# Kernel optimization log

Measured on AMD Instinct MI355X. Metric: run time of the kernel, lower is better.

## Reference

```python
import jax, jax.numpy as jnp
import numpy as np

NINP = 512
NHEAD = 8


def setup_inputs() -> dict:
    key = jax.random.key(0)
    ks = jax.random.split(key, 7)
    B, M, L, C = 2, 32, 512, NINP
    s = 1.0 / np.sqrt(C)
    return {
        "x": jax.random.normal(ks[0], (B, M, L, C), dtype=jnp.float32),
        "Wq": jax.random.normal(ks[1], (C, C), dtype=jnp.float32) * s,
        "bq": jax.random.normal(ks[2], (C,), dtype=jnp.float32) * s,
        "Wk": jax.random.normal(ks[3], (C, C), dtype=jnp.float32) * s,
        "bk": jax.random.normal(ks[4], (C,), dtype=jnp.float32) * s,
        "Wv": jax.random.normal(ks[5], (C, C), dtype=jnp.float32) * s,
        "bv": jax.random.normal(ks[6], (C,), dtype=jnp.float32) * s,
    }


def reference(x, Wq, bq, Wk, bk, Wv, bv) -> jnp.ndarray:
    # x: (B, M, L, C). Attention over L within each (B, M) block.
    B, M, L, C = x.shape
    H = NHEAD
    D = C // H
    scale = 1.0 / jnp.sqrt(jnp.asarray(D, dtype=x.dtype))

    def split_heads(t):  # (B,M,L,C) -> (B,M,H,L,D)
        return t.reshape(B, M, L, H, D).transpose(0, 1, 3, 2, 4)

    q = split_heads(x @ Wq + bq)
    k = split_heads(x @ Wk + bk)
    v = split_heads(x @ Wv + bv)

    scores = jnp.einsum("bmhid,bmhjd->bmhij", q, k) * scale
    w = jax.nn.softmax(scores, axis=-1)  # dropout p=0 -> identity
    out = jnp.einsum("bmhij,bmhjd->bmhid", w, v)  # (B,M,H,L,D)
    return out.transpose(0, 1, 3, 2, 4).reshape(B, M, L, C)
```

## Files before the change

### kernel.cpp

```cpp
#include <hip/hip_runtime.h>


typedef unsigned short u16;
typedef unsigned int u32;
typedef unsigned long long u64;
typedef __bf16 bf16x8 __attribute__((ext_vector_type(8)));
typedef float f32x4 __attribute__((ext_vector_type(4)));

#define SCQ 0.18033688011112042f

static __device__ __forceinline__ u16 f2bf(float f) {
  u32 x = __float_as_uint(f);
  x += 0x7fffu + ((x >> 16) & 1u);
  return (u16)(x >> 16);
}

static __device__ __forceinline__ u32 pkbf(float f0, float f1) {
  return __builtin_amdgcn_perm(__float_as_uint(f1) + 0x8000u,
                               __float_as_uint(f0) + 0x8000u, 0x07060302u);
}

typedef __attribute__((address_space(1))) const void* gvp;
typedef __attribute__((address_space(3))) void* lvp;
static __device__ __forceinline__ void glds16(const void* g, void* l) {
  __builtin_amdgcn_global_load_lds((gvp)g, (lvp)l, 16, 0, 0);
}

__global__ __launch_bounds__(256) void prep(const float* __restrict__ x,
                                            u16* __restrict__ xb,
                                            const float* __restrict__ Wq,
                                            const float* __restrict__ Wk,
                                            const float* __restrict__ Wv,
                                            u16* __restrict__ WT) {
  __shared__ float t[32][33];
  const int bx = blockIdx.x;
  if (bx < 8192) {
    const u32 i = (bx * 256u + threadIdx.x) * 8u;
    const float4 a = *(const float4*)(x + i);
    const float4 b = *(const float4*)(x + i + 4);
    union { u16 r[8]; uint4 v; } u;
    u.r[0] = f2bf(a.x); u.r[1] = f2bf(a.y); u.r[2] = f2bf(a.z); u.r[3] = f2bf(a.w);
    u.r[4] = f2bf(b.x); u.r[5] = f2bf(b.y); u.r[6] = f2bf(b.z); u.r[7] = f2bf(b.w);
    *(uint4*)(xb + i) = u.v;
    return;
  }
  const int b = bx - 8192;
  const int z = b >> 8;
  const int rem = b & 255;
  const float* W = (z == 0) ? Wq : ((z == 1) ? Wk : Wv);
  u16* dst = WT + z * 262144;
  const int k0 = (rem >> 4) * 32, n0 = (rem & 15) * 32;
  const int tx = threadIdx.x & 31, ty = threadIdx.x >> 5;
#pragma unroll
  for (int i = 0; i < 32; i += 8)
    t[ty + i][tx] = W[(size_t)(k0 + ty + i) * 512 + n0 + tx];
  __syncthreads();
#pragma unroll
  for (int i = 0; i < 32; i += 8)
    dst[(size_t)(n0 + ty + i) * 512 + k0 + tx] = f2bf(t[tx][ty + i]);
}

__global__ __launch_bounds__(256) void gemm_qkv(const u16* __restrict__ xb,
                                                const u16* __restrict__ WT,
                                                const float* __restrict__ bq,
                                                const float* __restrict__ bk,
                                                const float* __restrict__ bv,
                                                u16* __restrict__ qkv) {
  __shared__ __align__(16) u16 smem[24576];
  const int id = blockIdx.x;
  const int xcd = id & 7;
  const int slot = id >> 3;
  const int r12 = slot % 12;
  const int z = r12 >> 2;
  const int m = (slot / 12) * 8 + xcd;
  const int mbase = m * 128;
  const int nbase = (r12 & 3) * 128;
  const u16* Bg = WT + z * 262144;
  const float* bias = (z == 0) ? bq : ((z == 1) ? bk : bv);
  u16* out = qkv + (size_t)z * 16777216u;
  const int tid = threadIdx.x;
  const int lane = tid & 63;
  const int w = tid >> 6;
  const int wy = w >> 1, wx = w & 1;
  const int m15 = lane & 15, g = lane >> 4;

  const int srow = w * 32 + (lane >> 2);
  const int scol = (lane & 3) * 8;
  const u16* Ap = xb + (size_t)(mbase + srow) * 512 + scol;
  const u16* Bp = Bg + (size_t)(nbase + srow) * 512 + scol;

  f32x4 acc[4][4] = {};

#define STAGE(KT, B)                                  \
  do {                                                \
    const int k0_ = (KT) * 32;                        \
    u16* d_ = (B) + w * 1024;                         \
    glds16(Ap + k0_, d_);                             \
    glds16(Ap + k0_ + 16 * 512, d_ + 512);            \
    glds16(Bp + k0_, d_ + 4096);                      \
    glds16(Bp + k0_ + 16 * 512, d_ + 4096 + 512);     \
  } while (0)

#define COMPUTE(B)                                                          \
  do {                                                                      \
    bf16x8 af[4], bfr[4];                                                   \
    _Pragma("unroll") for (int t = 0; t < 4; ++t)                           \
        af[t] = *(const bf16x8*)&(B)[(wy * 64 + t * 16 + m15) * 32 + g * 8];\
    _Pragma("unroll") for (int t = 0; t < 4; ++t)                           \
        bfr[t] = *(const bf16x8*)&(B)[4096 + (wx * 64 + t * 16 + m15) * 32 + g * 8]; \
    _Pragma("unroll") for (int rt = 0; rt < 4; ++rt)                        \
        _Pragma("unroll") for (int ct = 0; ct < 4; ++ct)                    \
            acc[rt][ct] = __builtin_amdgcn_mfma_f32_16x16x32_bf16(          \
                af[rt], bfr[ct], acc[rt][ct], 0, 0, 0);                     \
  } while (0)

  STAGE(0, smem);
  STAGE(1, smem + 8192);
  STAGE(2, smem + 16384);

#pragma unroll
  for (int kt = 0; kt < 16; ++kt) {
    u16* cb = smem + (kt % 3) * 8192;
    if (kt < 14)
      asm volatile("s_waitcnt vmcnt(8)" ::: "memory");
    else if (kt == 14)
      asm volatile("s_waitcnt vmcnt(4)" ::: "memory");
    else
      asm volatile("s_waitcnt vmcnt(0)" ::: "memory");
    __builtin_amdgcn_s_barrier();
    COMPUTE(cb);
    asm volatile("s_waitcnt lgkmcnt(0)" ::: "memory");
    __builtin_amdgcn_s_barrier();
    if (kt + 3 < 16) STAGE(kt + 3, cb);
  }
#undef STAGE
#undef COMPUTE

  if (z < 2) {
    const float sc = (z == 0) ? SCQ : 1.0f;
#pragma unroll
    for (int ct = 0; ct < 4; ++ct) {
      const int col = nbase + wx * 64 + ct * 16 + m15;
      const float bb = bias[col];
#pragma unroll
      for (int rt = 0; rt < 4; ++rt) {
        const int row0 = mbase + wy * 64 + rt * 16 + g * 4;
#pragma unroll
        for (int r = 0; r < 4; ++r)
          out[(size_t)(row0 + r) * 512 + col] = f2bf((acc[rt][ct][r] + bb) * sc);
      }
    }
  } else {
    const int bm = mbase >> 9, jb = mbase & 511;
    u16* sT = smem;
#pragma unroll
    for (int cn = 0; cn < 4; ++cn) {
      __syncthreads();
      if (wx == (cn >> 1)) {
#pragma unroll
        for (int cte = 0; cte < 2; ++cte) {
          const int ct = (cn & 1) * 2 + cte;
          const int ncol = nbase + wx * 64 + ct * 16 + m15;
          const float bb = bias[ncol];
          const int nl = cte * 16 + m15;
#pragma unroll
          for (int rt = 0; rt < 4; ++rt) {
            u64 pk = 0;
#pragma unroll
            for (int r = 0; r < 4; ++r)
              pk |= (u64)f2bf(acc[rt][ct][r] + bb) << (16 * r);
            *(u64*)&sT[nl * 136 + wy * 64 + rt * 16 + g * 4] = pk;
          }
        }
      }
      __syncthreads();
#pragma unroll
      for (int it = 0; it < 2; ++it) {
        const int nl = it * 16 + (tid >> 4);
        const int ml = (tid & 15) * 8;
        const int ng = nbase + cn * 32 + nl;
        const int h = ng >> 6, d = ng & 63;
        *(uint4*)(out + ((size_t)((bm * 8 + h) * 64 + d)) * 512 + jb + ml) =
            *(const uint4*)&sT[nl * 136 + ml];
      }
    }
  }
}

__global__ __launch_bounds__(256) void attn(const u16* __restrict__ Q,
                                            const u16* __restrict__ K,
                                            const u16* __restrict__ Vt,
                                            float* __restrict__ out) {
  __shared__ __align__(16) char smem[36864];
  u16* sK = (u16*)smem;
  u16* sVT = (u16*)(smem + 9216);
  const int tid = threadIdx.x;
  const int lane = tid & 63;
  const int w = tid >> 6;
  const int m15 = lane & 15, g = lane >> 4;
  const int qt = blockIdx.x, h = blockIdx.y, bm = blockIdx.z;
  const size_t rb = (size_t)bm * 512;
  const int q0 = qt * 128 + w * 32;
  u16* sPT = (u16*)(smem + 18432) + w * 2304;

  bf16x8 qf[2][2];
#pragma unroll
  for (int ct = 0; ct < 2; ++ct)
#pragma unroll
    for (int kc = 0; kc < 2; ++kc)
      qf[ct][kc] =
          *(const bf16x8*)(Q + (rb + q0 + ct * 16 + m15) * 512 + h * 64 + kc * 32 + g * 8);

  f32x4 acc[4][2] = {};
  f32x4 lv[2] = {};

  const int srow = tid >> 3, sc8 = (tid & 7) * 8;
  const u16* Kb = K + rb * 512 + h * 64;
  const u16* Vtb = Vt + (size_t)(bm * 8 + h) * 64 * 512;

  uint4 k0v = *(const uint4*)(Kb + (size_t)srow * 512 + sc8);
  uint4 k1v = *(const uint4*)(Kb + (size_t)(srow + 32) * 512 + sc8);
  uint4 v0v = *(const uint4*)(Vtb + (size_t)srow * 512 + sc8);
  uint4 v1v = *(const uint4*)(Vtb + (size_t)(srow + 32) * 512 + sc8);

  for (int jt = 0; jt < 8; ++jt) {
    asm volatile("s_waitcnt lgkmcnt(0)" ::: "memory");
    __builtin_amdgcn_s_barrier();
    asm volatile("s_waitcnt vmcnt(0)" ::: "memory");
    *(uint4*)&sK[srow * 72 + sc8] = k0v;
    *(uint4*)&sK[(srow + 32) * 72 + sc8] = k1v;
    *(uint4*)&sVT[srow * 72 + sc8] = v0v;
    *(uint4*)&sVT[(srow + 32) * 72 + sc8] = v1v;
    if (jt < 7) {
      const int j1 = (jt + 1) * 64;
      k0v = *(const uint4*)(Kb + (size_t)(j1 + srow) * 512 + sc8);
      k1v = *(const uint4*)(Kb + (size_t)(j1 + srow + 32) * 512 + sc8);
      v0v = *(const uint4*)(Vtb + (size_t)srow * 512 + j1 + sc8);
      v1v = *(const uint4*)(Vtb + (size_t)(srow + 32) * 512 + j1 + sc8);
    }
    asm volatile("s_waitcnt lgkmcnt(0)" ::: "memory");
    __builtin_amdgcn_s_barrier();

    f32x4 s[4][2];
#pragma unroll
    for (int rt = 0; rt < 4; ++rt) {
      const bf16x8 k0 = *(const bf16x8*)&sK[(rt * 16 + m15) * 72 + g * 8];
      const bf16x8 k1 = *(const bf16x8*)&sK[(rt * 16 + m15) * 72 + 32 + g * 8];
#pragma unroll
      for (int ct = 0; ct < 2; ++ct) {
        f32x4 z = {};
        z = __builtin_amdgcn_mfma_f32_16x16x32_bf16(k0, qf[ct][0], z, 0, 0, 0);
        s[rt][ct] = __builtin_amdgcn_mfma_f32_16x16x32_bf16(k1, qf[ct][1], z, 0, 0, 0);
      }
    }

#pragma unroll
    for (int ct = 0; ct < 2; ++ct)
#pragma unroll
      for (int rt = 0; rt < 4; ++rt) {
        f32x4 p;
#pragma unroll
        for (int r = 0; r < 4; ++r) p[r] = exp2f(s[rt][ct][r]);
        lv[ct] += p;
        uint2 pk = {pkbf(p[0], p[1]), pkbf(p[2], p[3])};
        *(uint2*)&sPT[(ct * 16 + m15) * 72 + rt * 16 + g * 4] = pk;
      }

    bf16x8 pb[2][2];
#pragma unroll
    for (int ct = 0; ct < 2; ++ct)
#pragma unroll
      for (int kc = 0; kc < 2; ++kc)
        pb[ct][kc] = *(const bf16x8*)&sPT[(ct * 16 + m15) * 72 + kc * 32 + g * 8];
#pragma unroll
    for (int dt = 0; dt < 4; ++dt) {
      const bf16x8 v0 = *(const bf16x8*)&sVT[(dt * 16 + m15) * 72 + g * 8];
      const bf16x8 v1 = *(const bf16x8*)&sVT[(dt * 16 + m15) * 72 + 32 + g * 8];
#pragma unroll
      for (int ct = 0; ct < 2; ++ct) {
        acc[dt][ct] = __builtin_amdgcn_mfma_f32_16x16x32_bf16(v0, pb[ct][0], acc[dt][ct], 0, 0, 0);
        acc[dt][ct] = __builtin_amdgcn_mfma_f32_16x16x32_bf16(v1, pb[ct][1], acc[dt][ct], 0, 0, 0);
      }
    }
  }

  float inv[2];
#pragma unroll
  for (int ct = 0; ct < 2; ++ct) {
    float l = lv[ct][0] + lv[ct][1] + lv[ct][2] + lv[ct][3];
    l += __shfl_xor(l, 16);
    l += __shfl_xor(l, 32);
    inv[ct] = 1.0f / l;
  }
  __syncthreads();
  float* sO = (float*)(smem + w * 4608);
#pragma unroll
  for (int c = 0; c < 2; ++c) {
#pragma unroll
    for (int dt2 = 0; dt2 < 2; ++dt2)
#pragma unroll
      for (int ct = 0; ct < 2; ++ct) {
        f32x4 v = acc[c * 2 + dt2][ct] * inv[ct];
        *(f32x4*)&sO[(ct * 16 + m15) * 36 + dt2 * 16 + g * 4] = v;
      }
#pragma unroll
    for (int it = 0; it < 4; ++it) {
      const int q = it * 8 + (lane >> 3);
      f32x4 v = *(const f32x4*)&sO[q * 36 + (lane & 7) * 4];
      *(f32x4*)&out[(rb + q0 + q) * 512 + h * 64 + c * 32 + (lane & 7) * 4] = v;
    }
  }
}

extern "C" void kernel_launch(void* const* d_in, const int* in_sizes, int n_in,
                              void* d_out, int out_size, void* d_ws, size_t ws_size,
                              hipStream_t stream) {
  const float* x = (const float*)d_in[0];
  const float* Wq = (const float*)d_in[1];
  const float* bq = (const float*)d_in[2];
  const float* Wk = (const float*)d_in[3];
  const float* bk = (const float*)d_in[4];
  const float* Wv = (const float*)d_in[5];
  const float* bv = (const float*)d_in[6];
  float* out = (float*)d_out;

  u16* ws = (u16*)d_ws;
  u16* xb = ws;
  u16* WT = ws + 16777216;
  u16* qkv = ws + 17563648;

  prep<<<8960, 256, 0, stream>>>(x, xb, Wq, Wk, Wv, WT);
  gemm_qkv<<<3072, 256, 0, stream>>>(xb, WT, bq, bk, bv, qkv);
  attn<<<dim3(4, 8, 64), 256, 0, stream>>>(qkv, qkv + 16777216, qkv + 2 * 16777216, out);
}
```

Before: 256.0 us.

## Quad-buffer QKV GEMM, compute softmax sums via MFMA, remap attention grid

The QKV GEMM moves from three to four LDS stages, so the next tile's prefetch can be issued before compute and one barrier per k-step is dropped. In attention, the softmax row sums come from an MFMA against a ones vector on the bf16 probabilities instead of per-lane vector adds and cross-lane shuffles. The bf16 packing now uses the hardware v_cvt_pk_bf16_f32 instruction, and a 1D grid maps heads to adjacent block ids for better L2 locality on K and V. The costs are more LDS per GEMM block, which may lower occupancy, and normalising by the sum of bf16-rounded probabilities rather than the fp32 sum.

```diff
diff --git a/kernel.cpp b/kernel.cpp
--- a/kernel.cpp
+++ b/kernel.cpp
@@ -15,9 +15,10 @@
   return (u16)(x >> 16);
 }
 
-static __device__ __forceinline__ u32 pkbf(float f0, float f1) {
-  return __builtin_amdgcn_perm(__float_as_uint(f1) + 0x8000u,
-                               __float_as_uint(f0) + 0x8000u, 0x07060302u);
+static __device__ __forceinline__ u32 cvtpk(float lo, float hi) {
+  u32 r;
+  asm("v_cvt_pk_bf16_f32 %0, %1, %2" : "=v"(r) : "v"(lo), "v"(hi));
+  return r;
 }
 
 typedef __attribute__((address_space(1))) const void* gvp;
@@ -66,7 +67,7 @@
                                                 const float* __restrict__ bk,
                                                 const float* __restrict__ bv,
                                                 u16* __restrict__ qkv) {
-  __shared__ __align__(16) u16 smem[24576];
+  __shared__ __align__(16) u16 smem[32768];
   const int id = blockIdx.x;
   const int xcd = id & 7;
   const int slot = id >> 3;
@@ -120,7 +121,7 @@
 
 #pragma unroll
   for (int kt = 0; kt < 16; ++kt) {
-    u16* cb = smem + (kt % 3) * 8192;
+    u16* cb = smem + (kt & 3) * 8192;
     if (kt < 14)
       asm volatile("s_waitcnt vmcnt(8)" ::: "memory");
     else if (kt == 14)
@@ -128,10 +129,9 @@
     else
       asm volatile("s_waitcnt vmcnt(0)" ::: "memory");
     __builtin_amdgcn_s_barrier();
+    if (kt + 3 < 16) STAGE(kt + 3, smem + ((kt + 3) & 3) * 8192);
     COMPUTE(cb);
     asm volatile("s_waitcnt lgkmcnt(0)" ::: "memory");
-    __builtin_amdgcn_s_barrier();
-    if (kt + 3 < 16) STAGE(kt + 3, cb);
   }
 #undef STAGE
 #undef COMPUTE
@@ -198,7 +198,10 @@
   const int lane = tid & 63;
   const int w = tid >> 6;
   const int m15 = lane & 15, g = lane >> 4;
-  const int qt = blockIdx.x, h = blockIdx.y, bm = blockIdx.z;
+  const int id = blockIdx.x;
+  const int h = id & 7;
+  const int bm = id >> 5;
+  const int qt = (id >> 3) & 3;
   const size_t rb = (size_t)bm * 512;
   const int q0 = qt * 128 + w * 32;
   u16* sPT = (u16*)(smem + 18432) + w * 2304;
@@ -211,8 +214,12 @@
       qf[ct][kc] =
           *(const bf16x8*)(Q + (rb + q0 + ct * 16 + m15) * 512 + h * 64 + kc * 32 + g * 8);
 
+  bf16x8 ones;
+#pragma unroll
+  for (int i = 0; i < 8; ++i) ones[i] = (__bf16)1.0f;
+
   f32x4 acc[4][2] = {};
-  f32x4 lv[2] = {};
+  f32x4 accL[2] = {};
 
   const int srow = tid >> 3, sc8 = (tid & 7) * 8;
   const u16* Kb = K + rb * 512 + h * 64;
@@ -261,8 +268,7 @@
         f32x4 p;
 #pragma unroll
         for (int r = 0; r < 4; ++r) p[r] = exp2f(s[rt][ct][r]);
-        lv[ct] += p;
-        uint2 pk = {pkbf(p[0], p[1]), pkbf(p[2], p[3])};
+        uint2 pk = {cvtpk(p[0], p[1]), cvtpk(p[2], p[3])};
         *(uint2*)&sPT[(ct * 16 + m15) * 72 + rt * 16 + g * 4] = pk;
       }
 
@@ -272,6 +278,11 @@
 #pragma unroll
       for (int kc = 0; kc < 2; ++kc)
         pb[ct][kc] = *(const bf16x8*)&sPT[(ct * 16 + m15) * 72 + kc * 32 + g * 8];
+#pragma unroll
+    for (int ct = 0; ct < 2; ++ct) {
+      accL[ct] = __builtin_amdgcn_mfma_f32_16x16x32_bf16(ones, pb[ct][0], accL[ct], 0, 0, 0);
+      accL[ct] = __builtin_amdgcn_mfma_f32_16x16x32_bf16(ones, pb[ct][1], accL[ct], 0, 0, 0);
+    }
 #pragma unroll
     for (int dt = 0; dt < 4; ++dt) {
       const bf16x8 v0 = *(const bf16x8*)&sVT[(dt * 16 + m15) * 72 + g * 8];
@@ -286,12 +297,7 @@
 
   float inv[2];
 #pragma unroll
-  for (int ct = 0; ct < 2; ++ct) {
-    float l = lv[ct][0] + lv[ct][1] + lv[ct][2] + lv[ct][3];
-    l += __shfl_xor(l, 16);
-    l += __shfl_xor(l, 32);
-    inv[ct] = 1.0f / l;
-  }
+  for (int ct = 0; ct < 2; ++ct) inv[ct] = 1.0f / accL[ct][0];
   __syncthreads();
   float* sO = (float*)(smem + w * 4608);
 #pragma unroll
@@ -331,5 +337,5 @@
 
   prep<<<8960, 256, 0, stream>>>(x, xb, Wq, Wk, Wv, WT);
   gemm_qkv<<<3072, 256, 0, stream>>>(xb, WT, bq, bk, bv, qkv);
-  attn<<<dim3(4, 8, 64), 256, 0, stream>>>(qkv, qkv + 16777216, qkv + 2 * 16777216, out);
-}
+  attn<<<2048, 256, 0, stream>>>(qkv, qkv + 16777216, qkv + 2 * 16777216, out);
+}
```

Result: faster. 250.8 us (-2.0%).
